# Optimization experiments

Measured on AMD Instinct MI355X. Metric: run time of the kernel, lower is better.

The kernel has to match this reference:

```python
import jax, jax.numpy as jnp
import numpy as np

D_MODEL = 1024
H = 16
D_K = D_MODEL // H
B = 2
S = 2048


def setup_inputs() -> dict:
    key = jax.random.key(0)
    ks = jax.random.split(key, 13)
    scale = 1.0 / np.sqrt(D_MODEL)
    inp = {
        "Q": jax.random.normal(ks[0], (B, S, D_MODEL), jnp.float32),
        "K": jax.random.normal(ks[1], (B, S, D_MODEL), jnp.float32),
        "V": jax.random.normal(ks[2], (B, S, D_MODEL), jnp.float32),
        "mask": jax.random.randint(ks[3], (B, 1, S, S), 0, 2, jnp.int32),
        "WQ_w": jax.random.normal(ks[4], (D_MODEL, D_MODEL), jnp.float32) * scale,
        "WQ_b": jax.random.normal(ks[5], (D_MODEL,), jnp.float32) * scale,
        "WK_w": jax.random.normal(ks[6], (D_MODEL, D_MODEL), jnp.float32) * scale,
        "WK_b": jax.random.normal(ks[7], (D_MODEL,), jnp.float32) * scale,
        "WV_w": jax.random.normal(ks[8], (D_MODEL, D_MODEL), jnp.float32) * scale,
        "WV_b": jax.random.normal(ks[9], (D_MODEL,), jnp.float32) * scale,
        "WO_w": jax.random.normal(ks[10], (D_MODEL, D_MODEL), jnp.float32) * scale,
        "WO_b": jax.random.normal(ks[11], (D_MODEL,), jnp.float32) * scale,
    }
    return inp


def _split_heads(x):
    # [B,S,D] -> [B,H,S,d_k]
    b, s, _ = x.shape
    return x.reshape(b, s, H, D_K).transpose(0, 2, 1, 3)


def reference(Q, K, V, mask, WQ_w, WQ_b, WK_w, WK_b, WV_w, WV_b, WO_w, WO_b):
    q = _split_heads(Q @ WQ_w.T + WQ_b)
    k = _split_heads(K @ WK_w.T + WK_b)
    v = _split_heads(V @ WV_w.T + WV_b)
    scores = jnp.einsum("bhqd,bhkd->bhqk", q, k) / jnp.sqrt(jnp.float32(D_K))
    # NOTE: original code fills masked positions with 1e-9 (not -inf) -- replicate faithfully
    scores = jnp.where(mask == 0, jnp.float32(1e-9), scores)
    attn = jax.nn.softmax(scores, axis=-1)
    out = jnp.einsum("bhqk,bhkd->bhqd", attn, v)  # [B,H,S,d_k]
    out = out.transpose(0, 2, 1, 3).reshape(Q.shape[0], -1, D_MODEL)
    return out @ WO_w.T + WO_b
```

## Files before the change

kernel.cpp:

```cpp
#include <hip/hip_runtime.h>
#include <stdint.h>

#define D_MODEL 1024
#define NH 16
#define DKK 64
#define SEQ 2048
#define QSCALE 0.18033688011112042f

using half8 = __attribute__((ext_vector_type(8))) _Float16;
using half4 = __attribute__((ext_vector_type(4))) _Float16;
using half2v = __attribute__((ext_vector_type(2))) _Float16;
using fp16x2 = __attribute__((ext_vector_type(2))) __fp16;
using f32x4 = __attribute__((ext_vector_type(4))) float;

__device__ __forceinline__ f32x4 fz4() { f32x4 v = {0.f, 0.f, 0.f, 0.f}; return v; }

__device__ __forceinline__ void gload16(const void* g, void* l) {
    __builtin_amdgcn_global_load_lds(
        (const __attribute__((address_space(1))) unsigned int*)g,
        (__attribute__((address_space(3))) unsigned int*)l, 16, 0, 0);
}

__device__ __forceinline__ half2v pk2(float a, float b) {
    fp16x2 t = __builtin_amdgcn_cvt_pkrtz(a, b);
    return __builtin_bit_cast(half2v, t);
}

__device__ __forceinline__ half4 pk4(float a, float b, float c, float d) {
    half2v lo = pk2(a, b);
    half2v hi = pk2(c, d);
    half4 r; r.x = lo.x; r.y = lo.y; r.z = hi.x; r.w = hi.y;
    return r;
}

__device__ __forceinline__ int xswz(int bid, int n) {
    return (bid & 7) * (n >> 3) + (bid >> 3);
}

__global__ __launch_bounds__(256) void conv_all(const float* __restrict__ wq,
                                                const float* __restrict__ wk,
                                                const float* __restrict__ wv,
                                                const float* __restrict__ wo,
                                                const float* __restrict__ Q,
                                                const float* __restrict__ K,
                                                const float* __restrict__ V,
                                                _Float16* __restrict__ out) {
    int idx = blockIdx.x * 256 + threadIdx.x;
#pragma unroll
    for (int k = 0; k < 8; ++k) {
        int c = idx + k * 524288;
        const float* src;
        int off;
        if (c < 1048576) {
            int w = c >> 18;
            src = (w == 0) ? wq : (w == 1) ? wk : (w == 2) ? wv : wo;
            off = c & 0x3ffff;
        } else {
            int j = (c >> 20) - 1;
            src = (j == 0) ? Q : (j == 1) ? K : V;
            off = c & 0xfffff;
        }
        float4 v = ((const float4*)src)[off];
        ((half4*)out)[c] = pk4(v.x, v.y, v.z, v.w);
    }
}

__global__ __launch_bounds__(256) void pack_mask_k(const int* __restrict__ mask,
                                                   unsigned int* __restrict__ mbits) {
    int wid = threadIdx.x >> 6, lane = threadIdx.x & 63;
    int row = blockIdx.x * 4 + wid;
    const int* mrow = mask + (size_t)row * SEQ;
    unsigned int* orow = mbits + (size_t)row * (SEQ / 32);
    for (int it = 0; it < SEQ / 64; ++it) {
        int v = mrow[it * 64 + lane];
        unsigned long long bal = __ballot(v != 0);
        if (lane == 0)       orow[it * 2]     = (unsigned int)(bal & 0xffffffffull);
        else if (lane == 32) orow[it * 2 + 1] = (unsigned int)(bal >> 32);
    }
}

__device__ __forceinline__ void gemm_body(const _Float16* __restrict__ A,
                                          const _Float16* __restrict__ Wh,
                                          const float* __restrict__ bias,
                                          void* __restrict__ outp, int omode, float scale) {
    __shared__ __align__(16) _Float16 Asm[2][64 * 64];
    __shared__ __align__(16) _Float16 Bsm[2][128 * 64];
    const int tid = threadIdx.x;
    const int wg = xswz(blockIdx.x, 512);
    const int bm = wg >> 3, bn = wg & 7;
    const int wid = tid >> 6, lane = tid & 63;
    const int li = lane & 15, g = lane >> 4;
    const int wm = wid >> 1, wn = wid & 1;

    const int brow = wid * 32 + (lane >> 3);
    const char* bsrc = (const char*)(Wh + (size_t)(bn * 128 + brow) * D_MODEL)
                       + (((lane & 7) ^ (brow & 7)) * 16);
    const int bdst = wid * 32 * 128;
    const int arow = wid * 16 + (lane >> 3);
    const char* asrc = (const char*)(A + (size_t)(bm * 64 + arow) * D_MODEL)
                       + (((lane & 7) ^ (arow & 7)) * 16);
    const int adst = wid * 16 * 128;

    f32x4 acc[2][4];
#pragma unroll
    for (int i = 0; i < 2; ++i)
#pragma unroll
        for (int j = 0; j < 4; ++j) acc[i][j] = fz4();

    const int o0 = ((g << 4))      ^ ((li & 7) << 4);
    const int o1 = (64 + (g << 4)) ^ ((li & 7) << 4);
    const int abase = wm * 4096 + li * 128;
    const int bbase = wn * 8192 + li * 128;

    auto stage = [&](int it, int buf) {
        const char* bs = bsrc + it * 128;
        char* bd = (char*)&Bsm[buf][0] + bdst;
        gload16(bs,             bd);
        gload16(bs +  8 * 2048, bd + 1024);
        gload16(bs + 16 * 2048, bd + 2048);
        gload16(bs + 24 * 2048, bd + 3072);
        const char* as = asrc + it * 128;
        char* ad = (char*)&Asm[buf][0] + adst;
        gload16(as,            ad);
        gload16(as + 8 * 2048, ad + 1024);
    };

    stage(0, 0);
    __syncthreads();

    for (int it = 0; it < 16; ++it) {
        const int cur = it & 1;
        if (it + 1 < 16) stage(it + 1, cur ^ 1);
        const char* ab = (const char*)&Asm[cur][0];
        const char* bb = (const char*)&Bsm[cur][0];
#pragma unroll
        for (int s = 0; s < 2; ++s) {
            const int oS = s ? o1 : o0;
            half8 af0 = *(const half8*)(ab + abase + 0    + oS);
            half8 af1 = *(const half8*)(ab + abase + 2048 + oS);
            half8 bf[4];
#pragma unroll
            for (int nt = 0; nt < 4; ++nt)
                bf[nt] = *(const half8*)(bb + bbase + nt * 2048 + oS);
#pragma unroll
            for (int nt = 0; nt < 4; ++nt) {
                acc[0][nt] = __builtin_amdgcn_mfma_f32_16x16x32_f16(af0, bf[nt], acc[0][nt], 0, 0, 0);
                acc[1][nt] = __builtin_amdgcn_mfma_f32_16x16x32_f16(af1, bf[nt], acc[1][nt], 0, 0, 0);
            }
        }
        __syncthreads();
    }

#pragma unroll
    for (int nt = 0; nt < 4; ++nt) {
        int n = bn * 128 + wn * 64 + nt * 16 + li;
        float bv = bias[n];
#pragma unroll
        for (int mt = 0; mt < 2; ++mt) {
            if (omode == 1) {
                int s0 = bm * 64 + wm * 32 + mt * 16 + g * 4;
                int b = (bm * 64) >> 11;
                int h = n >> 6, d = n & 63;
                half4 hv = pk4(acc[mt][nt][0] + bv, acc[mt][nt][1] + bv,
                               acc[mt][nt][2] + bv, acc[mt][nt][3] + bv);
                *(half4*)((_Float16*)outp +
                          ((((size_t)(b * NH + h)) * DKK + d) * SEQ + (s0 & (SEQ - 1)))) = hv;
            } else {
#pragma unroll
                for (int r = 0; r < 4; ++r) {
                    int m = bm * 64 + wm * 32 + mt * 16 + g * 4 + r;
                    float val = (acc[mt][nt][r] + bv) * scale;
                    if (omode == 2) {
                        ((float*)outp)[(size_t)m * D_MODEL + n] = val;
                    } else {
                        int b = m >> 11, s = m & (SEQ - 1);
                        int h = n >> 6, d = n & 63;
                        ((_Float16*)outp)[(((size_t)(b * NH + h)) * SEQ + s) * DKK + d] =
                            (_Float16)val;
                    }
                }
            }
        }
    }
}

struct QkvArgs {
    const float *b0, *b1, *b2;
    _Float16 *o0, *o1, *o2;
};

__global__ __launch_bounds__(256) void gemm_qkv(const _Float16* __restrict__ Ah,
                                                const _Float16* __restrict__ cw,
                                                QkvArgs ga) {
    const int z = blockIdx.y;
    const _Float16* A  = Ah + (size_t)z * (D_MODEL * 4096);
    const float* bi = (z == 0) ? ga.b0 : (z == 1) ? ga.b1 : ga.b2;
    _Float16*    o  = (z == 0) ? ga.o0 : (z == 1) ? ga.o1 : ga.o2;
    gemm_body(A, cw + (size_t)z * D_MODEL * D_MODEL, bi, o,
              (z == 2) ? 1 : 0, (z == 0) ? QSCALE : 1.0f);
}

__global__ __launch_bounds__(256) void gemm_out(const _Float16* __restrict__ A,
                                                const _Float16* __restrict__ cw,
                                                const float* __restrict__ bias,
                                                float* __restrict__ out) {
    gemm_body(A, cw, bias, out, 2, 1.0f);
}

__global__ __launch_bounds__(256, 4) void attn_fwd(const _Float16* __restrict__ q,
                                                   const _Float16* __restrict__ kk,
                                                   const _Float16* __restrict__ vt,
                                                   const unsigned int* __restrict__ mb,
                                                   _Float16* __restrict__ aout) {
    __shared__ __align__(16) _Float16 klds[2][64 * 64];
    __shared__ __align__(16) _Float16 vlds[2][64 * 64];
    __shared__ __align__(16) _Float16 plds[4][16 * 64];
    const int wg = xswz(blockIdx.x, 1024);
    const int qblk = wg & 31, bh = wg >> 5;
    const int b = bh >> 4, h = bh & 15;
    const int tid = threadIdx.x, wid = tid >> 6, lane = tid & 63;
    const int li = lane & 15, g = lane >> 4;
    const _Float16* qp = q  + (size_t)bh * SEQ * DKK;
    const _Float16* kp = kk + (size_t)bh * SEQ * DKK;
    const _Float16* vp = vt + (size_t)bh * DKK * SEQ;
    const int qrow0 = qblk * 64 + wid * 16;

    half8 qf[2];
#pragma unroll
    for (int s = 0; s < 2; ++s)
        qf[s] = *(const half8*)(qp + (size_t)(qrow0 + li) * DKK + s * 32 + g * 8);

    half8 ones;
#pragma unroll
    for (int j = 0; j < 8; ++j) ones[j] = (_Float16)1.0f;

    const int srow = wid * 16 + (lane >> 3);
    const int sswz = ((lane & 7) ^ (srow & 7)) * 16;
    const char* ksrc = (const char*)(kp + (size_t)srow * DKK) + sswz;
    const char* vsrc = (const char*)(vp + (size_t)srow * SEQ) + sswz;
    const int sdst = wid * 2048;

    auto stage = [&](int it, int buf) {
        const char* ks = ksrc + (size_t)it * 8192;
        const char* vs = vsrc + (size_t)it * 128;
        char* kd = (char*)&klds[buf][0] + sdst;
        char* vd = (char*)&vlds[buf][0] + sdst;
        gload16(ks,                       kd);
        gload16(ks + 8 * 128,             kd + 1024);
        gload16(vs,                       vd);
        gload16(vs + 8 * (size_t)SEQ * 2, vd + 1024);
    };

    f32x4 O[4];
#pragma unroll
    for (int dt = 0; dt < 4; ++dt) O[dt] = fz4();
    f32x4 Ol = fz4();

    const unsigned int* m0 = mb + ((size_t)b * SEQ + qrow0 + li) * (SEQ / 32);

    char* pw = (char*)&plds[wid][0];
    const int pswz = (li & 7) << 4;
    const int prow = li * 128;

    const int o0 = ((g << 4))      ^ ((li & 7) << 4);
    const int o1 = (64 + (g << 4)) ^ ((li & 7) << 4);
    const int kfb = li * 128;

    stage(0, 0);
    __syncthreads();

    for (int it = 0; it < SEQ / 64; ++it) {
        const int cur = it & 1;
        if (it + 1 < SEQ / 64) stage(it + 1, cur ^ 1);
        uint2 ma = *(const uint2*)(m0 + it * 2);

        f32x4 st[4];
#pragma unroll
        for (int t = 0; t < 4; ++t) st[t] = fz4();
        const char* kb_ = (const char*)&klds[cur][0];
        __builtin_amdgcn_s_setprio(1);
#pragma unroll
        for (int t = 0; t < 4; ++t) {
            half8 kf0 = *(const half8*)(kb_ + kfb + t * 2048 + o0);
            half8 kf1 = *(const half8*)(kb_ + kfb + t * 2048 + o1);
            st[t] = __builtin_amdgcn_mfma_f32_16x16x32_f16(kf0, qf[0], st[t], 0, 0, 0);
            st[t] = __builtin_amdgcn_mfma_f32_16x16x32_f16(kf1, qf[1], st[t], 0, 0, 0);
        }
        __builtin_amdgcn_s_setprio(0);

#pragma unroll
        for (int t = 0; t < 4; ++t) {
            unsigned wsel = ((t < 2) ? ma.x : ma.y) >> (g * 4);
            const int sh = (t & 1) << 4;
            float e0 = __builtin_amdgcn_exp2f(st[t][0]);
            float e1 = __builtin_amdgcn_exp2f(st[t][1]);
            float e2 = __builtin_amdgcn_exp2f(st[t][2]);
            float e3 = __builtin_amdgcn_exp2f(st[t][3]);
            float p0 = ((wsel >> (sh + 0)) & 1u) ? e0 : 1.0f;
            float p1 = ((wsel >> (sh + 1)) & 1u) ? e1 : 1.0f;
            float p2 = ((wsel >> (sh + 2)) & 1u) ? e2 : 1.0f;
            float p3 = ((wsel >> (sh + 3)) & 1u) ? e3 : 1.0f;
            *(half4*)(pw + prow + ((t * 32 + g * 8) ^ pswz)) = pk4(p0, p1, p2, p3);
        }

        half8 pB[2];
#pragma unroll
        for (int s = 0; s < 2; ++s)
            pB[s] = *(const half8*)(pw + prow + ((s * 64 + g * 16) ^ pswz));
        const char* vb_ = (const char*)&vlds[cur][0];
        __builtin_amdgcn_s_setprio(1);
        Ol = __builtin_amdgcn_mfma_f32_16x16x32_f16(ones, pB[0], Ol, 0, 0, 0);
        Ol = __builtin_amdgcn_mfma_f32_16x16x32_f16(ones, pB[1], Ol, 0, 0, 0);
#pragma unroll
        for (int dt = 0; dt < 4; ++dt) {
            half8 vf0 = *(const half8*)(vb_ + kfb + dt * 2048 + o0);
            half8 vf1 = *(const half8*)(vb_ + kfb + dt * 2048 + o1);
            O[dt] = __builtin_amdgcn_mfma_f32_16x16x32_f16(vf0, pB[0], O[dt], 0, 0, 0);
            O[dt] = __builtin_amdgcn_mfma_f32_16x16x32_f16(vf1, pB[1], O[dt], 0, 0, 0);
        }
        __builtin_amdgcn_s_setprio(0);
        __syncthreads();
    }

    float inv = 1.0f / Ol[0];
    _Float16* orow = aout + ((size_t)(b * SEQ + qrow0 + li)) * D_MODEL + h * DKK + g * 4;
#pragma unroll
    for (int dt = 0; dt < 4; ++dt)
        *(half4*)(orow + dt * 16) = pk4(O[dt][0] * inv, O[dt][1] * inv,
                                        O[dt][2] * inv, O[dt][3] * inv);
}

extern "C" void kernel_launch(void* const* d_in, const int* in_sizes, int n_in,
                              void* d_out, int out_size, void* d_ws, size_t ws_size,
                              hipStream_t stream) {
    const float* Q    = (const float*)d_in[0];
    const float* Kin  = (const float*)d_in[1];
    const float* Vin  = (const float*)d_in[2];
    const int*   mask = (const int*)d_in[3];
    const float* WQw = (const float*)d_in[4];
    const float* WQb = (const float*)d_in[5];
    const float* WKw = (const float*)d_in[6];
    const float* WKb = (const float*)d_in[7];
    const float* WVw = (const float*)d_in[8];
    const float* WVb = (const float*)d_in[9];
    const float* WOw = (const float*)d_in[10];
    const float* WOb = (const float*)d_in[11];

    char* w = (char*)d_ws;
    const size_t MB = 1ull << 20;
    _Float16* cw  = (_Float16*)(w);
    _Float16* Ah  = (_Float16*)(w + 8 * MB);
    _Float16* ab  = (_Float16*)(w + 8 * MB);
    _Float16* qb  = (_Float16*)(w + 32 * MB);
    _Float16* kbf = (_Float16*)(w + 40 * MB);
    _Float16* vtb = (_Float16*)(w + 48 * MB);
    unsigned int* mbits = (unsigned int*)(w + 56 * MB);

    conv_all<<<dim3(2048), dim3(256), 0, stream>>>(WQw, WKw, WVw, WOw, Q, Kin, Vin, cw);
    pack_mask_k<<<dim3(1024), dim3(256), 0, stream>>>(mask, mbits);

    QkvArgs ga;
    ga.b0 = WQb; ga.b1 = WKb; ga.b2 = WVb;
    ga.o0 = qb;  ga.o1 = kbf; ga.o2 = vtb;
    gemm_qkv<<<dim3(512, 3), dim3(256), 0, stream>>>(Ah, cw, ga);

    attn_fwd<<<dim3(1024), dim3(256), 0, stream>>>(qb, kbf, vtb, mbits, ab);

    gemm_out<<<dim3(512), dim3(256), 0, stream>>>(ab, cw + 3ull * D_MODEL * D_MODEL, WOb,
                                                  (float*)d_out);
}
```

Baseline: 144.4 us.

## Fuse activation fp16 conversion into QKV GEMM and drop LDS staging in attention

```diff
diff --git a/kernel.cpp b/kernel.cpp
--- a/kernel.cpp
+++ b/kernel.cpp
@@ -37,30 +37,18 @@
     return (bid & 7) * (n >> 3) + (bid >> 3);
 }
 
-__global__ __launch_bounds__(256) void conv_all(const float* __restrict__ wq,
-                                                const float* __restrict__ wk,
-                                                const float* __restrict__ wv,
-                                                const float* __restrict__ wo,
-                                                const float* __restrict__ Q,
-                                                const float* __restrict__ K,
-                                                const float* __restrict__ V,
-                                                _Float16* __restrict__ out) {
+__global__ __launch_bounds__(256) void conv_w(const float* __restrict__ wq,
+                                              const float* __restrict__ wk,
+                                              const float* __restrict__ wv,
+                                              const float* __restrict__ wo,
+                                              _Float16* __restrict__ out) {
     int idx = blockIdx.x * 256 + threadIdx.x;
 #pragma unroll
-    for (int k = 0; k < 8; ++k) {
+    for (int k = 0; k < 2; ++k) {
         int c = idx + k * 524288;
-        const float* src;
-        int off;
-        if (c < 1048576) {
-            int w = c >> 18;
-            src = (w == 0) ? wq : (w == 1) ? wk : (w == 2) ? wv : wo;
-            off = c & 0x3ffff;
-        } else {
-            int j = (c >> 20) - 1;
-            src = (j == 0) ? Q : (j == 1) ? K : V;
-            off = c & 0xfffff;
-        }
-        float4 v = ((const float4*)src)[off];
+        int w = c >> 18;
+        const float* src = (w == 0) ? wq : (w == 1) ? wk : (w == 2) ? wv : wo;
+        float4 v = ((const float4*)src)[c & 0x3ffff];
         ((half4*)out)[c] = pk4(v.x, v.y, v.z, v.w);
     }
 }
@@ -79,7 +67,8 @@
     }
 }
 
-__device__ __forceinline__ void gemm_body(const _Float16* __restrict__ A,
+template <int AMODE>
+__device__ __forceinline__ void gemm_body(const void* __restrict__ Ap,
                                           const _Float16* __restrict__ Wh,
                                           const float* __restrict__ bias,
                                           void* __restrict__ outp, int omode, float scale) {
@@ -96,10 +85,15 @@
     const char* bsrc = (const char*)(Wh + (size_t)(bn * 128 + brow) * D_MODEL)
                        + (((lane & 7) ^ (brow & 7)) * 16);
     const int bdst = wid * 32 * 128;
-    const int arow = wid * 16 + (lane >> 3);
-    const char* asrc = (const char*)(A + (size_t)(bm * 64 + arow) * D_MODEL)
-                       + (((lane & 7) ^ (arow & 7)) * 16);
-    const int adst = wid * 16 * 128;
+
+    const int arow0 = wid * 16 + (lane >> 2);
+    const float* asrc4 = (const float*)Ap + (size_t)(bm * 64 + arow0) * D_MODEL + (lane & 3) * 16;
+    const int awo0 = arow0 * 128 + (((lane & 3) * 32)      ^ ((arow0 & 7) << 4));
+    const int awo1 = arow0 * 128 + (((lane & 3) * 32 + 16) ^ ((arow0 & 7) << 4));
+    const int arow1 = wid * 16 + (lane >> 3);
+    const char* asrc1 = (const char*)Ap + (size_t)(bm * 64 + arow1) * (D_MODEL * 2)
+                        + (((lane & 7) ^ (arow1 & 7)) * 16);
+    const int adst1 = wid * 16 * 128;
 
     f32x4 acc[2][4];
 #pragma unroll
@@ -119,10 +113,26 @@
         gload16(bs +  8 * 2048, bd + 1024);
         gload16(bs + 16 * 2048, bd + 2048);
         gload16(bs + 24 * 2048, bd + 3072);
-        const char* as = asrc + it * 128;
-        char* ad = (char*)&Asm[buf][0] + adst;
-        gload16(as,            ad);
-        gload16(as + 8 * 2048, ad + 1024);
+        if constexpr (AMODE == 0) {
+            const float* s = asrc4 + it * 64;
+            float4 v0 = *(const float4*)(s);
+            float4 v1 = *(const float4*)(s + 4);
+            float4 v2 = *(const float4*)(s + 8);
+            float4 v3 = *(const float4*)(s + 12);
+            char* d = (char*)&Asm[buf][0];
+            half8 h0, h1;
+            *(half4*)&h0 = pk4(v0.x, v0.y, v0.z, v0.w);
+            *((half4*)&h0 + 1) = pk4(v1.x, v1.y, v1.z, v1.w);
+            *(half4*)&h1 = pk4(v2.x, v2.y, v2.z, v2.w);
+            *((half4*)&h1 + 1) = pk4(v3.x, v3.y, v3.z, v3.w);
+            *(half8*)(d + awo0) = h0;
+            *(half8*)(d + awo1) = h1;
+        } else {
+            const char* as = asrc1 + it * 128;
+            char* ad = (char*)&Asm[buf][0] + adst1;
+            gload16(as,            ad);
+            gload16(as + 8 * 2048, ad + 1024);
+        }
     };
 
     stage(0, 0);
@@ -185,26 +195,24 @@
 }
 
 struct QkvArgs {
-    const float *b0, *b1, *b2;
+    const float *A0, *A1, *A2, *b0, *b1, *b2;
     _Float16 *o0, *o1, *o2;
 };
 
-__global__ __launch_bounds__(256) void gemm_qkv(const _Float16* __restrict__ Ah,
-                                                const _Float16* __restrict__ cw,
-                                                QkvArgs ga) {
+__global__ __launch_bounds__(256) void gemm_qkv(QkvArgs ga, const _Float16* __restrict__ cw) {
     const int z = blockIdx.y;
-    const _Float16* A  = Ah + (size_t)z * (D_MODEL * 4096);
+    const float* A  = (z == 0) ? ga.A0 : (z == 1) ? ga.A1 : ga.A2;
     const float* bi = (z == 0) ? ga.b0 : (z == 1) ? ga.b1 : ga.b2;
     _Float16*    o  = (z == 0) ? ga.o0 : (z == 1) ? ga.o1 : ga.o2;
-    gemm_body(A, cw + (size_t)z * D_MODEL * D_MODEL, bi, o,
-              (z == 2) ? 1 : 0, (z == 0) ? QSCALE : 1.0f);
+    gemm_body<0>(A, cw + (size_t)z * D_MODEL * D_MODEL, bi, o,
+                 (z == 2) ? 1 : 0, (z == 0) ? QSCALE : 1.0f);
 }
 
 __global__ __launch_bounds__(256) void gemm_out(const _Float16* __restrict__ A,
                                                 const _Float16* __restrict__ cw,
                                                 const float* __restrict__ bias,
                                                 float* __restrict__ out) {
-    gemm_body(A, cw, bias, out, 2, 1.0f);
+    gemm_body<1>(A, cw, bias, out, 2, 1.0f);
 }
 
 __global__ __launch_bounds__(256, 4) void attn_fwd(const _Float16* __restrict__ q,
@@ -212,8 +220,6 @@
                                                    const _Float16* __restrict__ vt,
                                                    const unsigned int* __restrict__ mb,
                                                    _Float16* __restrict__ aout) {
-    __shared__ __align__(16) _Float16 klds[2][64 * 64];
-    __shared__ __align__(16) _Float16 vlds[2][64 * 64];
     __shared__ __align__(16) _Float16 plds[4][16 * 64];
     const int wg = xswz(blockIdx.x, 1024);
     const int qblk = wg & 31, bh = wg >> 5;
@@ -234,23 +240,6 @@
 #pragma unroll
     for (int j = 0; j < 8; ++j) ones[j] = (_Float16)1.0f;
 
-    const int srow = wid * 16 + (lane >> 3);
-    const int sswz = ((lane & 7) ^ (srow & 7)) * 16;
-    const char* ksrc = (const char*)(kp + (size_t)srow * DKK) + sswz;
-    const char* vsrc = (const char*)(vp + (size_t)srow * SEQ) + sswz;
-    const int sdst = wid * 2048;
-
-    auto stage = [&](int it, int buf) {
-        const char* ks = ksrc + (size_t)it * 8192;
-        const char* vs = vsrc + (size_t)it * 128;
-        char* kd = (char*)&klds[buf][0] + sdst;
-        char* vd = (char*)&vlds[buf][0] + sdst;
-        gload16(ks,                       kd);
-        gload16(ks + 8 * 128,             kd + 1024);
-        gload16(vs,                       vd);
-        gload16(vs + 8 * (size_t)SEQ * 2, vd + 1024);
-    };
-
     f32x4 O[4];
 #pragma unroll
     for (int dt = 0; dt < 4; ++dt) O[dt] = fz4();
@@ -262,31 +251,34 @@
     const int pswz = (li & 7) << 4;
     const int prow = li * 128;
 
-    const int o0 = ((g << 4))      ^ ((li & 7) << 4);
-    const int o1 = (64 + (g << 4)) ^ ((li & 7) << 4);
-    const int kfb = li * 128;
-
-    stage(0, 0);
-    __syncthreads();
+    const _Float16* kfp = kp + (size_t)li * DKK + g * 8;
+    const _Float16* vfp = vp + (size_t)li * SEQ + g * 8;
 
     for (int it = 0; it < SEQ / 64; ++it) {
-        const int cur = it & 1;
-        if (it + 1 < SEQ / 64) stage(it + 1, cur ^ 1);
+        const int kb = it * 64;
         uint2 ma = *(const uint2*)(m0 + it * 2);
 
         f32x4 st[4];
 #pragma unroll
         for (int t = 0; t < 4; ++t) st[t] = fz4();
-        const char* kb_ = (const char*)&klds[cur][0];
         __builtin_amdgcn_s_setprio(1);
 #pragma unroll
         for (int t = 0; t < 4; ++t) {
-            half8 kf0 = *(const half8*)(kb_ + kfb + t * 2048 + o0);
-            half8 kf1 = *(const half8*)(kb_ + kfb + t * 2048 + o1);
+            const _Float16* kr = kfp + (size_t)(kb + t * 16) * DKK;
+            half8 kf0 = *(const half8*)(kr);
+            half8 kf1 = *(const half8*)(kr + 32);
             st[t] = __builtin_amdgcn_mfma_f32_16x16x32_f16(kf0, qf[0], st[t], 0, 0, 0);
             st[t] = __builtin_amdgcn_mfma_f32_16x16x32_f16(kf1, qf[1], st[t], 0, 0, 0);
         }
         __builtin_amdgcn_s_setprio(0);
+
+        half8 vf[4][2];
+#pragma unroll
+        for (int dt = 0; dt < 4; ++dt) {
+            const _Float16* vr = vfp + (size_t)(dt * 16) * SEQ + kb;
+            vf[dt][0] = *(const half8*)(vr);
+            vf[dt][1] = *(const half8*)(vr + 32);
+        }
 
 #pragma unroll
         for (int t = 0; t < 4; ++t) {
@@ -307,19 +299,15 @@
 #pragma unroll
         for (int s = 0; s < 2; ++s)
             pB[s] = *(const half8*)(pw + prow + ((s * 64 + g * 16) ^ pswz));
-        const char* vb_ = (const char*)&vlds[cur][0];
         __builtin_amdgcn_s_setprio(1);
         Ol = __builtin_amdgcn_mfma_f32_16x16x32_f16(ones, pB[0], Ol, 0, 0, 0);
         Ol = __builtin_amdgcn_mfma_f32_16x16x32_f16(ones, pB[1], Ol, 0, 0, 0);
 #pragma unroll
         for (int dt = 0; dt < 4; ++dt) {
-            half8 vf0 = *(const half8*)(vb_ + kfb + dt * 2048 + o0);
-            half8 vf1 = *(const half8*)(vb_ + kfb + dt * 2048 + o1);
-            O[dt] = __builtin_amdgcn_mfma_f32_16x16x32_f16(vf0, pB[0], O[dt], 0, 0, 0);
-            O[dt] = __builtin_amdgcn_mfma_f32_16x16x32_f16(vf1, pB[1], O[dt], 0, 0, 0);
+            O[dt] = __builtin_amdgcn_mfma_f32_16x16x32_f16(vf[dt][0], pB[0], O[dt], 0, 0, 0);
+            O[dt] = __builtin_amdgcn_mfma_f32_16x16x32_f16(vf[dt][1], pB[1], O[dt], 0, 0, 0);
         }
         __builtin_amdgcn_s_setprio(0);
-        __syncthreads();
     }
 
     float inv = 1.0f / Ol[0];
@@ -349,20 +337,20 @@
     char* w = (char*)d_ws;
     const size_t MB = 1ull << 20;
     _Float16* cw  = (_Float16*)(w);
-    _Float16* Ah  = (_Float16*)(w + 8 * MB);
     _Float16* ab  = (_Float16*)(w + 8 * MB);
-    _Float16* qb  = (_Float16*)(w + 32 * MB);
-    _Float16* kbf = (_Float16*)(w + 40 * MB);
-    _Float16* vtb = (_Float16*)(w + 48 * MB);
-    unsigned int* mbits = (unsigned int*)(w + 56 * MB);
-
-    conv_all<<<dim3(2048), dim3(256), 0, stream>>>(WQw, WKw, WVw, WOw, Q, Kin, Vin, cw);
+    _Float16* qb  = (_Float16*)(w + 16 * MB);
+    _Float16* kbf = (_Float16*)(w + 24 * MB);
+    _Float16* vtb = (_Float16*)(w + 32 * MB);
+    unsigned int* mbits = (unsigned int*)(w + 40 * MB);
+
+    conv_w<<<dim3(2048), dim3(256), 0, stream>>>(WQw, WKw, WVw, WOw, cw);
     pack_mask_k<<<dim3(1024), dim3(256), 0, stream>>>(mask, mbits);
 
     QkvArgs ga;
+    ga.A0 = Q;   ga.A1 = Kin; ga.A2 = Vin;
     ga.b0 = WQb; ga.b1 = WKb; ga.b2 = WVb;
     ga.o0 = qb;  ga.o1 = kbf; ga.o2 = vtb;
-    gemm_qkv<<<dim3(512, 3), dim3(256), 0, stream>>>(Ah, cw, ga);
+    gemm_qkv<<<dim3(512, 3), dim3(256), 0, stream>>>(ga, cw);
 
     attn_fwd<<<dim3(1024), dim3(256), 0, stream>>>(qb, kbf, vtb, mbits, ab);
 
```

New measurement: 327.5 us. +126.7%, slower.
